# Kernel optimization log

Hardware: AMD Instinct MI355X
Metric: run time of the kernel (lower is better)

Reference implementation:

```python
import jax, jax.numpy as jnp
import numpy as np

CLASS_COUNT = 21
THRESHOLD = 0.5
ALPHA = 0.25
GAMMA = 2.0
VARIANCE = (0.1, 0.2)

B, A, N_OBJ = 32, 24576, 16


def point_form(boxes):
    # center form (cx, cy, w, h) -> point form (xmin, ymin, xmax, ymax)
    return jnp.concatenate([boxes[:, :2] - boxes[:, 2:] / 2,
                            boxes[:, :2] + boxes[:, 2:] / 2], axis=1)


def jaccard(truths, priors):
    # truths [N,4], priors [A,4] both in point form -> IoU [N, A]
    lt = jnp.maximum(truths[:, None, :2], priors[None, :, :2])
    rb = jnp.minimum(truths[:, None, 2:], priors[None, :, 2:])
    wh = jnp.clip(rb - lt, 0.0, None)
    inter = wh[..., 0] * wh[..., 1]
    area_t = ((truths[:, 2] - truths[:, 0]) * (truths[:, 3] - truths[:, 1]))[:, None]
    area_p = ((priors[:, 2] - priors[:, 0]) * (priors[:, 3] - priors[:, 1]))[None, :]
    return inter / (area_t + area_p - inter)


def match_one(labels, truths, anchors):
    # labels [N] int, truths [N,4] point form, anchors [A,4] center form
    overlaps = jaccard(truths, point_form(anchors))           # [N, A]
    best_prior_idx = jnp.argmax(overlaps, axis=1)             # [N]
    best_truth_overlap = jnp.max(overlaps, axis=0)            # [A]
    best_truth_idx = jnp.argmax(overlaps, axis=0)             # [A]
    # ensure every gt matches its best prior
    best_truth_overlap = best_truth_overlap.at[best_prior_idx].set(2.0)
    best_truth_idx = best_truth_idx.at[best_prior_idx].set(jnp.arange(truths.shape[0]))
    matches = truths[best_truth_idx]                          # [A, 4]
    conf = jnp.where(best_truth_overlap < THRESHOLD, 0, labels[best_truth_idx])
    # encode with variances
    g_cxcy = ((matches[:, :2] + matches[:, 2:]) * 0.5 - anchors[:, :2]) / (VARIANCE[0] * anchors[:, 2:])
    g_wh = jnp.log((matches[:, 2:] - matches[:, :2]) / anchors[:, 2:]) / VARIANCE[1]
    return conf, jnp.concatenate([g_cxcy, g_wh], axis=1)


def setup_inputs() -> dict:
    key = jax.random.key(0)
    k1, k2, k3, k4, k5, k6, k7 = jax.random.split(key, 7)
    class_preds = jax.random.normal(k1, (B, A, CLASS_COUNT), dtype=jnp.float32)
    loc_preds = jax.random.normal(k2, (B, A, 4), dtype=jnp.float32)
    # ground-truth boxes: random valid point-form boxes in [0,1]
    ctr = jax.random.uniform(k3, (B, N_OBJ, 2), minval=0.2, maxval=0.8)
    wh = jax.random.uniform(k4, (B, N_OBJ, 2), minval=0.05, maxval=0.3)
    loc_targets = jnp.clip(jnp.concatenate([ctr - wh / 2, ctr + wh / 2], axis=-1), 0.0, 1.0)
    class_targets = jax.random.randint(k5, (B, N_OBJ), 1, CLASS_COUNT)
    # anchors in center form
    a_ctr = jax.random.uniform(k6, (A, 2), minval=0.05, maxval=0.95)
    a_wh = jax.random.uniform(k7, (A, 2), minval=0.05, maxval=0.4)
    anchors = jnp.concatenate([a_ctr, a_wh], axis=1)
    return {"class_preds": class_preds, "loc_preds": loc_preds,
            "loc_targets": loc_targets, "anchors": anchors,
            "class_targets": class_targets}


def reference(class_preds, loc_preds, loc_targets, anchors, class_targets):
    conf, loc_t = jax.vmap(match_one, in_axes=(0, 0, None))(class_targets, loc_targets, anchors)
    pos = conf > 0                                            # [B, A]
    num_matched = jnp.sum(pos).astype(jnp.float32)
    # smooth L1 over positive anchors (sum reduction, beta=1)
    d = loc_preds - loc_t
    ad = jnp.abs(d)
    sl1 = jnp.where(ad < 1.0, 0.5 * d * d, ad - 0.5)
    loc_loss = jnp.sum(sl1 * pos[..., None].astype(sl1.dtype))
    # focal loss (drop background column 0)
    cp = class_preds.reshape(-1, CLASS_COUNT)[:, 1:]          # [B*A, C-1]
    t = jax.nn.one_hot(conf.reshape(-1), CLASS_COUNT, dtype=cp.dtype)[:, 1:]
    p = jax.nn.sigmoid(cp)
    pt = jnp.where(t > 0, p, 1.0 - p)
    w = (1.0 - pt) ** GAMMA
    w = jnp.where(t > 0, ALPHA * w, (1.0 - ALPHA) * w)
    # stable binary cross entropy with logits, weighted, sum reduction
    bce = jnp.maximum(cp, 0.0) - cp * t + jnp.log1p(jnp.exp(-jnp.abs(cp)))
    class_loss = jnp.sum(w * bce)
    class_loss = class_loss / num_matched
    loc_loss = loc_loss / num_matched
    return jnp.stack([class_loss, loc_loss, class_loss + loc_loss])
```

## Files before the change

### kernel.cpp

```cpp
#include <hip/hip_runtime.h>

#define A_COUNT 24576
#define B_COUNT 32
#define NOBJ 16
#define C_COUNT 21

#define NCH 96
#define CHUNK (A_COUNT / NCH)
#define NBLK (NCH * B_COUNT)
#define TOTAL4 (B_COUNT * A_COUNT * C_COUNT / 4)
#define STRIDE4 (NBLK * 256)

#define WS_BPP 0
#define WS_LOCP 393216
#define WS_CLSP 405504
#define WS_POSP 417792
#define WS_DLOC 430080
#define WS_DCLS 430208
#define WS_DPOS 430336

__device__ __forceinline__ unsigned long long pack_key(float iou, int a) {
    unsigned int ib = __float_as_uint(iou);
    return ((unsigned long long)ib << 32) | (unsigned long long)(0xFFFFFFFFu - (unsigned int)a);
}

__device__ __forceinline__ float iou_pf(float tx0, float ty0, float tx1, float ty1, float at,
                                        float x0, float y0, float x1, float y1, float ap) {
    float lx = fmaxf(tx0, x0), ly = fmaxf(ty0, y0);
    float rx = fminf(tx1, x1), ry = fminf(ty1, y1);
    float w = fmaxf(rx - lx, 0.0f), h = fmaxf(ry - ly, 0.0f);
    float inter = w * h;
    return inter * __builtin_amdgcn_rcpf(at + ap - inter);
}

__device__ __forceinline__ float sl1(float d) {
    float ad = fabsf(d);
    return (ad < 1.0f) ? 0.5f * d * d : ad - 0.5f;
}

__device__ __forceinline__ float loc_term(float4 t, float4 an, float4 lp) {
    float gx = ((t.x + t.z) * 0.5f - an.x) / (0.1f * an.z);
    float gy = ((t.y + t.w) * 0.5f - an.y) / (0.1f * an.w);
    float gw = __logf((t.z - t.x) / an.z) * 5.0f;
    float gh = __logf((t.w - t.y) / an.w) * 5.0f;
    return sl1(lp.x - gx) + sl1(lp.y - gy) + sl1(lp.z - gw) + sl1(lp.w - gh);
}

__device__ __forceinline__ float corr_term(float x) {
    float E = __expf(x);
    float den = 1.0f + E;
    float s = __builtin_amdgcn_rcpf(den);
    float p = E * s;
    float L = __logf(den);
    return 0.25f * s * s * (L - x) - 0.75f * p * p * L;
}

#define FOC(xval, rr, acc) {                                 \
    float E_ = __expf(xval);                                 \
    float den_ = 1.0f + E_;                                  \
    float s_ = __builtin_amdgcn_rcpf(den_);                  \
    float p_ = E_ * s_;                                      \
    float L_ = __logf(den_);                                 \
    float v_ = ((rr) == 0 || (rr) == 21) ? 0.0f : p_ * p_ * L_; \
    acc += v_; }

__global__ __launch_bounds__(256, 4) void k_main(const float* __restrict__ cls,
                                                 const float4* __restrict__ locp,
                                                 const float4* __restrict__ anchors,
                                                 const float4* __restrict__ truths,
                                                 const int* __restrict__ labels,
                                                 unsigned long long* __restrict__ bp_partial,
                                                 float* __restrict__ loc_partial,
                                                 float* __restrict__ cls_partial,
                                                 unsigned int* __restrict__ pos_partial) {
    const int ch = blockIdx.x;
    const int b = blockIdx.y;
    const int tid = threadIdx.x;
    __shared__ float4 s_t[NOBJ];
    __shared__ float s_area[NOBJ];
    __shared__ int s_lab[NOBJ];
    __shared__ unsigned long long s_keys[8][256];
    if (tid < NOBJ) {
        float4 t = truths[b * NOBJ + tid];
        s_t[tid] = t;
        s_area[tid] = (t.z - t.x) * (t.w - t.y);
        s_lab[tid] = labels[b * NOBJ + tid];
    }
    __syncthreads();
    const int a0 = ch * CHUNK + tid;
    float4 an0 = anchors[a0];
    float p0x0 = an0.x - an0.z * 0.5f, p0y0 = an0.y - an0.w * 0.5f;
    float p0x1 = an0.x + an0.z * 0.5f, p0y1 = an0.y + an0.w * 0.5f;
    float ap0 = (p0x1 - p0x0) * (p0y1 - p0y0);
    float best0 = -1.0f;
    int idx0 = 0;
#pragma unroll
    for (int half = 0; half < 2; ++half) {
#pragma unroll
        for (int n = 0; n < 8; ++n) {
            const int nt = half * 8 + n;
            float4 t = s_t[nt];
            float at = s_area[nt];
            float iou0 = iou_pf(t.x, t.y, t.z, t.w, at, p0x0, p0y0, p0x1, p0y1, ap0);
            if (iou0 > best0) { best0 = iou0; idx0 = nt; }
            s_keys[n][tid] = pack_key(iou0, a0);
        }
        __syncthreads();
        if (tid < 128) {
            const int g = tid >> 4, l = tid & 15;
            unsigned long long k = s_keys[g][l];
#pragma unroll
            for (int kk = 1; kk < 16; ++kk) {
                unsigned long long v = s_keys[g][l + 16 * kk];
                k = (v > k) ? v : k;
            }
#pragma unroll
            for (int s = 8; s >= 1; s >>= 1) {
                unsigned long long o = __shfl_xor(k, s);
                k = (o > k) ? o : k;
            }
            if (l == 0) bp_partial[(b * NOBJ + half * 8 + g) * NCH + ch] = k;
        }
        __syncthreads();
    }
    float loc_l = 0.0f, corr_acc = 0.0f;
    unsigned int pos = 0;
    if (!(best0 < 0.5f)) {
        pos = 1;
        loc_l = loc_term(s_t[idx0], an0, locp[(size_t)b * A_COUNT + a0]);
        corr_acc = corr_term(cls[((size_t)b * A_COUNT + a0) * C_COUNT + s_lab[idx0]]);
    }

    const int bid = b * NCH + ch;
    float cls_acc;
    {
        const float4* cls4 = (const float4*)cls;
        int i = bid * 256 + tid;
        unsigned int f = (unsigned int)i * 4u;
        unsigned int dq = f / 21u;
        int r = (int)(f - dq * 21u);
        float acc0 = 0.0f, acc1 = 0.0f, acc2 = 0.0f, acc3 = 0.0f;
        for (; i < TOTAL4; i += STRIDE4) {
            float4 x4 = cls4[i];
            FOC(x4.x, r + 0, acc0); FOC(x4.y, r + 1, acc1);
            FOC(x4.z, r + 2, acc2); FOC(x4.w, r + 3, acc3);
            r += 12; if (r >= 21) r -= 21;
        }
        cls_acc = corr_acc + 0.75f * ((acc0 + acc1) + (acc2 + acc3));
    }

#pragma unroll
    for (int s = 32; s >= 1; s >>= 1) {
        loc_l += __shfl_xor(loc_l, s);
        cls_acc += __shfl_xor(cls_acc, s);
        pos += __shfl_xor(pos, s);
    }
    __shared__ float s_ll[4], s_cl[4];
    __shared__ unsigned int s_pp[4];
    if ((tid & 63) == 0) {
        s_ll[tid >> 6] = loc_l;
        s_cl[tid >> 6] = cls_acc;
        s_pp[tid >> 6] = pos;
    }
    __syncthreads();
    if (tid == 0) {
        loc_partial[bid] = s_ll[0] + s_ll[1] + s_ll[2] + s_ll[3];
        cls_partial[bid] = s_cl[0] + s_cl[1] + s_cl[2] + s_cl[3];
        pos_partial[bid] = s_pp[0] + s_pp[1] + s_pp[2] + s_pp[3];
    }
}

__global__ __launch_bounds__(256) void k_fix(const float* __restrict__ cls,
                                             const float4* __restrict__ locp,
                                             const float4* __restrict__ anchors,
                                             const float4* __restrict__ truths,
                                             const int* __restrict__ labels,
                                             const unsigned long long* __restrict__ bp_partial,
                                             float* __restrict__ dloc,
                                             float* __restrict__ dcls,
                                             int* __restrict__ dpos) {
    const int b = blockIdx.x;
    const int tid = threadIdx.x;
    __shared__ int s_bp[NOBJ];
    {
        const int g = tid >> 4, l = tid & 15;
        const unsigned long long* pp = &bp_partial[(size_t)(b * NOBJ + g) * NCH];
        unsigned long long k = pp[l];
#pragma unroll
        for (int kk = 1; kk < 6; ++kk) {
            unsigned long long v = pp[l + 16 * kk];
            k = (v > k) ? v : k;
        }
#pragma unroll
        for (int s = 8; s >= 1; s >>= 1) {
            unsigned long long o = __shfl_xor(k, s);
            k = (o > k) ? o : k;
        }
        if (l == 0) {
            unsigned int ia = 0xFFFFFFFFu - (unsigned int)(k & 0xFFFFFFFFull);
            s_bp[g] = (ia >= A_COUNT) ? -1 : (int)ia;
        }
    }
    __syncthreads();
    float d_loc = 0.0f, d_cls = 0.0f;
    int d_pos = 0;
    if (tid < NOBJ) {
        const int n = tid;
        const int q = s_bp[n];
        bool winner = (q >= 0);
        for (int n2 = n + 1; n2 < NOBJ; ++n2)
            if (s_bp[n2] == q) winner = false;
        if (winner) {
            float4 an = anchors[q];
            float px0 = an.x - an.z * 0.5f, py0 = an.y - an.w * 0.5f;
            float px1 = an.x + an.z * 0.5f, py1 = an.y + an.w * 0.5f;
            float ap = (px1 - px0) * (py1 - py0);
            float best = -1.0f;
            int idx = 0;
            for (int n2 = 0; n2 < NOBJ; ++n2) {
                float4 t = truths[b * NOBJ + n2];
                float at = (t.z - t.x) * (t.w - t.y);
                float iou = iou_pf(t.x, t.y, t.z, t.w, at, px0, py0, px1, py1, ap);
                if (iou > best) { best = iou; idx = n2; }
            }
            float4 lp = locp[(size_t)b * A_COUNT + q];
            if (!(best < 0.5f)) {
                d_pos -= 1;
                d_loc -= loc_term(truths[b * NOBJ + idx], an, lp);
                d_cls -= corr_term(cls[((size_t)b * A_COUNT + q) * C_COUNT + labels[b * NOBJ + idx]]);
            }
            d_pos += 1;
            d_loc += loc_term(truths[b * NOBJ + n], an, lp);
            d_cls += corr_term(cls[((size_t)b * A_COUNT + q) * C_COUNT + labels[b * NOBJ + n]]);
        }
    }
    if (tid < 64) {
#pragma unroll
        for (int s = 8; s >= 1; s >>= 1) {
            d_loc += __shfl_xor(d_loc, s);
            d_cls += __shfl_xor(d_cls, s);
            d_pos += __shfl_xor(d_pos, s);
        }
        if (tid == 0) {
            dloc[b] = d_loc;
            dcls[b] = d_cls;
            dpos[b] = d_pos;
        }
    }
}

__global__ __launch_bounds__(256) void k_final(const float* __restrict__ loc_partial,
                                               const float* __restrict__ cls_partial,
                                               const unsigned int* __restrict__ pos_partial,
                                               const float* __restrict__ dloc,
                                               const float* __restrict__ dcls,
                                               const int* __restrict__ dpos,
                                               float* __restrict__ out) {
    const int tid = threadIdx.x;
    double loc = 0.0, clsv = 0.0;
    int pos = 0;
    for (int i = tid; i < NBLK; i += 256) {
        loc += (double)loc_partial[i];
        clsv += (double)cls_partial[i];
        pos += (int)pos_partial[i];
    }
    if (tid < B_COUNT) {
        loc += (double)dloc[tid];
        clsv += (double)dcls[tid];
        pos += dpos[tid];
    }
#pragma unroll
    for (int s = 32; s >= 1; s >>= 1) {
        loc += __shfl_xor(loc, s);
        clsv += __shfl_xor(clsv, s);
        pos += __shfl_xor(pos, s);
    }
    __shared__ double s_l[4], s_c[4];
    __shared__ int s_p[4];
    if ((tid & 63) == 0) {
        s_l[tid >> 6] = loc;
        s_c[tid >> 6] = clsv;
        s_p[tid >> 6] = pos;
    }
    __syncthreads();
    if (tid == 0) {
        double L = s_l[0] + s_l[1] + s_l[2] + s_l[3];
        double Cv = s_c[0] + s_c[1] + s_c[2] + s_c[3];
        float nm = (float)(s_p[0] + s_p[1] + s_p[2] + s_p[3]);
        float cf = (float)Cv / nm;
        float lf = (float)L / nm;
        out[0] = cf;
        out[1] = lf;
        out[2] = cf + lf;
    }
}

extern "C" void kernel_launch(void* const* d_in, const int* in_sizes, int n_in,
                              void* d_out, int out_size, void* d_ws, size_t ws_size,
                              hipStream_t stream) {
    const float* cls = (const float*)d_in[0];
    const float4* locp = (const float4*)d_in[1];
    const float4* truths = (const float4*)d_in[2];
    const float4* anchors = (const float4*)d_in[3];
    const int* labels = (const int*)d_in[4];

    char* ws = (char*)d_ws;
    unsigned long long* bp_partial = (unsigned long long*)(ws + WS_BPP);
    float* loc_partial = (float*)(ws + WS_LOCP);
    float* cls_partial = (float*)(ws + WS_CLSP);
    unsigned int* pos_partial = (unsigned int*)(ws + WS_POSP);
    float* dloc = (float*)(ws + WS_DLOC);
    float* dcls = (float*)(ws + WS_DCLS);
    int* dpos = (int*)(ws + WS_DPOS);

    k_main<<<dim3(NCH, B_COUNT), 256, 0, stream>>>(cls, locp, anchors, truths, labels,
                                                   bp_partial, loc_partial, cls_partial, pos_partial);
    k_fix<<<B_COUNT, 256, 0, stream>>>(cls, locp, anchors, truths, labels, bp_partial,
                                       dloc, dcls, dpos);
    k_final<<<1, 256, 0, stream>>>(loc_partial, cls_partial, pos_partial, dloc, dcls, dpos,
                                   (float*)d_out);
}
```

Before: 41.65 us.

## Replace shared-memory key reduction with wave shuffle argmax and raise occupancy

The per-truth best-anchor reduction, which staged 64-bit keys in a 16KB shared array with two barrier rounds per half, becomes a wavefront shuffle max plus ballot to pick the first lane holding the maximum. Each wave writes one key per truth to a small shared array and 16 threads combine the four waves. This removes most shared-memory traffic and barriers and shrinks LDS use, and launch bounds are raised to 8 blocks per SM to allow more occupancy. The lowest-lane tie break assumes lane order matches anchor order so the smallest anchor index wins, and the higher occupancy target may limit registers for the focal-loss loop.

```diff
diff --git a/kernel.cpp b/kernel.cpp
--- a/kernel.cpp
+++ b/kernel.cpp
@@ -64,7 +64,7 @@
     float v_ = ((rr) == 0 || (rr) == 21) ? 0.0f : p_ * p_ * L_; \
     acc += v_; }
 
-__global__ __launch_bounds__(256, 4) void k_main(const float* __restrict__ cls,
+__global__ __launch_bounds__(256, 8) void k_main(const float* __restrict__ cls,
                                                  const float4* __restrict__ locp,
                                                  const float4* __restrict__ anchors,
                                                  const float4* __restrict__ truths,
@@ -76,10 +76,11 @@
     const int ch = blockIdx.x;
     const int b = blockIdx.y;
     const int tid = threadIdx.x;
+    const int wv = tid >> 6, ln = tid & 63;
     __shared__ float4 s_t[NOBJ];
     __shared__ float s_area[NOBJ];
     __shared__ int s_lab[NOBJ];
-    __shared__ unsigned long long s_keys[8][256];
+    __shared__ unsigned long long s_w[NOBJ][4];
     if (tid < NOBJ) {
         float4 t = truths[b * NOBJ + tid];
         s_t[tid] = t;
@@ -95,33 +96,23 @@
     float best0 = -1.0f;
     int idx0 = 0;
 #pragma unroll
-    for (int half = 0; half < 2; ++half) {
-#pragma unroll
-        for (int n = 0; n < 8; ++n) {
-            const int nt = half * 8 + n;
-            float4 t = s_t[nt];
-            float at = s_area[nt];
-            float iou0 = iou_pf(t.x, t.y, t.z, t.w, at, p0x0, p0y0, p0x1, p0y1, ap0);
-            if (iou0 > best0) { best0 = iou0; idx0 = nt; }
-            s_keys[n][tid] = pack_key(iou0, a0);
-        }
-        __syncthreads();
-        if (tid < 128) {
-            const int g = tid >> 4, l = tid & 15;
-            unsigned long long k = s_keys[g][l];
-#pragma unroll
-            for (int kk = 1; kk < 16; ++kk) {
-                unsigned long long v = s_keys[g][l + 16 * kk];
-                k = (v > k) ? v : k;
-            }
-#pragma unroll
-            for (int s = 8; s >= 1; s >>= 1) {
-                unsigned long long o = __shfl_xor(k, s);
-                k = (o > k) ? o : k;
-            }
-            if (l == 0) bp_partial[(b * NOBJ + half * 8 + g) * NCH + ch] = k;
-        }
-        __syncthreads();
+    for (int n = 0; n < NOBJ; ++n) {
+        float4 t = s_t[n];
+        float iou = iou_pf(t.x, t.y, t.z, t.w, s_area[n], p0x0, p0y0, p0x1, p0y1, ap0);
+        if (iou > best0) { best0 = iou; idx0 = n; }
+        float m = iou;
+#pragma unroll
+        for (int s = 32; s >= 1; s >>= 1) m = fmaxf(m, __shfl_xor(m, s));
+        unsigned long long mask = __ballot(iou == m);
+        if (ln == __builtin_ctzll(mask))
+            s_w[n][wv] = pack_key(iou, a0);
+    }
+    __syncthreads();
+    if (tid < NOBJ) {
+        unsigned long long k = s_w[tid][0];
+#pragma unroll
+        for (int i = 1; i < 4; ++i) k = (s_w[tid][i] > k) ? s_w[tid][i] : k;
+        bp_partial[(b * NOBJ + tid) * NCH + ch] = k;
     }
     float loc_l = 0.0f, corr_acc = 0.0f;
     unsigned int pos = 0;
@@ -157,10 +148,10 @@
     }
     __shared__ float s_ll[4], s_cl[4];
     __shared__ unsigned int s_pp[4];
-    if ((tid & 63) == 0) {
-        s_ll[tid >> 6] = loc_l;
-        s_cl[tid >> 6] = cls_acc;
-        s_pp[tid >> 6] = pos;
+    if (ln == 0) {
+        s_ll[wv] = loc_l;
+        s_cl[wv] = cls_acc;
+        s_pp[wv] = pos;
     }
     __syncthreads();
     if (tid == 0) {
```

Measured after the change: 48.85 us. +17.3%, slower.

## Merge fix-up and final reduction into one tail kernel; prefetch focal loads

Applied to the files above, without the earlier changes.

Replaces the per-batch fix-up kernel and the final reduction kernel with a single one-block tail kernel. It performs the best-prior argmax for all 512 rows, applies the forced-match corrections, and sums all partials, which removes one kernel launch and the workspace round trip. The focal-loss streaming loop in the main kernel now software-prefetches the next float4 before computing on the current one, to hide load latency. The cost is that the fix-up work is serialized into a single block instead of 32.

```diff
diff --git a/kernel.cpp b/kernel.cpp
--- a/kernel.cpp
+++ b/kernel.cpp
@@ -8,6 +8,7 @@
 #define NCH 96
 #define CHUNK (A_COUNT / NCH)
 #define NBLK (NCH * B_COUNT)
+#define NROWS (B_COUNT * NOBJ)
 #define TOTAL4 (B_COUNT * A_COUNT * C_COUNT / 4)
 #define STRIDE4 (NBLK * 256)
 
@@ -15,9 +16,6 @@
 #define WS_LOCP 393216
 #define WS_CLSP 405504
 #define WS_POSP 417792
-#define WS_DLOC 430080
-#define WS_DCLS 430208
-#define WS_DPOS 430336
 
 __device__ __forceinline__ unsigned long long pack_key(float iou, int a) {
     unsigned int ib = __float_as_uint(iou);
@@ -140,10 +138,17 @@
         unsigned int dq = f / 21u;
         int r = (int)(f - dq * 21u);
         float acc0 = 0.0f, acc1 = 0.0f, acc2 = 0.0f, acc3 = 0.0f;
-        for (; i < TOTAL4; i += STRIDE4) {
-            float4 x4 = cls4[i];
-            FOC(x4.x, r + 0, acc0); FOC(x4.y, r + 1, acc1);
-            FOC(x4.z, r + 2, acc2); FOC(x4.w, r + 3, acc3);
+        float4 cur = cls4[i];
+        for (;;) {
+            const int inext = i + STRIDE4;
+            const bool more = inext < TOTAL4;
+            float4 nxt;
+            if (more) nxt = cls4[inext];
+            FOC(cur.x, r + 0, acc0); FOC(cur.y, r + 1, acc1);
+            FOC(cur.z, r + 2, acc2); FOC(cur.w, r + 3, acc3);
+            if (!more) break;
+            cur = nxt;
+            i = inext;
             r += 12; if (r >= 21) r -= 21;
         }
         cls_acc = corr_acc + 0.75f * ((acc0 + acc1) + (acc2 + acc3));
@@ -170,104 +175,80 @@
     }
 }
 
-__global__ __launch_bounds__(256) void k_fix(const float* __restrict__ cls,
-                                             const float4* __restrict__ locp,
-                                             const float4* __restrict__ anchors,
-                                             const float4* __restrict__ truths,
-                                             const int* __restrict__ labels,
-                                             const unsigned long long* __restrict__ bp_partial,
-                                             float* __restrict__ dloc,
-                                             float* __restrict__ dcls,
-                                             int* __restrict__ dpos) {
-    const int b = blockIdx.x;
+__global__ __launch_bounds__(256) void k_tail(const float* __restrict__ cls,
+                                              const float4* __restrict__ locp,
+                                              const float4* __restrict__ anchors,
+                                              const float4* __restrict__ truths,
+                                              const int* __restrict__ labels,
+                                              const unsigned long long* __restrict__ bp_partial,
+                                              const float* __restrict__ loc_partial,
+                                              const float* __restrict__ cls_partial,
+                                              const unsigned int* __restrict__ pos_partial,
+                                              float* __restrict__ out) {
     const int tid = threadIdx.x;
-    __shared__ int s_bp[NOBJ];
+    __shared__ int s_bp[NROWS];
     {
         const int g = tid >> 4, l = tid & 15;
-        const unsigned long long* pp = &bp_partial[(size_t)(b * NOBJ + g) * NCH];
-        unsigned long long k = pp[l];
-#pragma unroll
-        for (int kk = 1; kk < 6; ++kk) {
-            unsigned long long v = pp[l + 16 * kk];
-            k = (v > k) ? v : k;
-        }
-#pragma unroll
-        for (int s = 8; s >= 1; s >>= 1) {
-            unsigned long long o = __shfl_xor(k, s);
-            k = (o > k) ? o : k;
-        }
-        if (l == 0) {
-            unsigned int ia = 0xFFFFFFFFu - (unsigned int)(k & 0xFFFFFFFFull);
-            s_bp[g] = (ia >= A_COUNT) ? -1 : (int)ia;
-        }
-    }
-    __syncthreads();
+        for (int base = 0; base < NROWS; base += 16) {
+            const int row = base + g;
+            const unsigned long long* pp = &bp_partial[(size_t)row * NCH];
+            unsigned long long k = pp[l];
+#pragma unroll
+            for (int kk = 1; kk < 6; ++kk) {
+                unsigned long long v = pp[l + 16 * kk];
+                k = (v > k) ? v : k;
+            }
+#pragma unroll
+            for (int s = 8; s >= 1; s >>= 1) {
+                unsigned long long o = __shfl_xor(k, s);
+                k = (o > k) ? o : k;
+            }
+            if (l == 0) {
+                unsigned int ia = 0xFFFFFFFFu - (unsigned int)(k & 0xFFFFFFFFull);
+                s_bp[row] = (ia >= A_COUNT) ? -1 : (int)ia;
+            }
+        }
+    }
+    __syncthreads();
+
     float d_loc = 0.0f, d_cls = 0.0f;
     int d_pos = 0;
-    if (tid < NOBJ) {
-        const int n = tid;
-        const int q = s_bp[n];
+    for (int pr = tid; pr < NROWS; pr += 256) {
+        const int b2 = pr >> 4, n = pr & 15;
+        const int q = s_bp[pr];
         bool winner = (q >= 0);
         for (int n2 = n + 1; n2 < NOBJ; ++n2)
-            if (s_bp[n2] == q) winner = false;
-        if (winner) {
-            float4 an = anchors[q];
-            float px0 = an.x - an.z * 0.5f, py0 = an.y - an.w * 0.5f;
-            float px1 = an.x + an.z * 0.5f, py1 = an.y + an.w * 0.5f;
-            float ap = (px1 - px0) * (py1 - py0);
-            float best = -1.0f;
-            int idx = 0;
-            for (int n2 = 0; n2 < NOBJ; ++n2) {
-                float4 t = truths[b * NOBJ + n2];
-                float at = (t.z - t.x) * (t.w - t.y);
-                float iou = iou_pf(t.x, t.y, t.z, t.w, at, px0, py0, px1, py1, ap);
-                if (iou > best) { best = iou; idx = n2; }
-            }
-            float4 lp = locp[(size_t)b * A_COUNT + q];
-            if (!(best < 0.5f)) {
-                d_pos -= 1;
-                d_loc -= loc_term(truths[b * NOBJ + idx], an, lp);
-                d_cls -= corr_term(cls[((size_t)b * A_COUNT + q) * C_COUNT + labels[b * NOBJ + idx]]);
-            }
-            d_pos += 1;
-            d_loc += loc_term(truths[b * NOBJ + n], an, lp);
-            d_cls += corr_term(cls[((size_t)b * A_COUNT + q) * C_COUNT + labels[b * NOBJ + n]]);
-        }
-    }
-    if (tid < 64) {
-#pragma unroll
-        for (int s = 8; s >= 1; s >>= 1) {
-            d_loc += __shfl_xor(d_loc, s);
-            d_cls += __shfl_xor(d_cls, s);
-            d_pos += __shfl_xor(d_pos, s);
-        }
-        if (tid == 0) {
-            dloc[b] = d_loc;
-            dcls[b] = d_cls;
-            dpos[b] = d_pos;
-        }
-    }
-}
-
-__global__ __launch_bounds__(256) void k_final(const float* __restrict__ loc_partial,
-                                               const float* __restrict__ cls_partial,
-                                               const unsigned int* __restrict__ pos_partial,
-                                               const float* __restrict__ dloc,
-                                               const float* __restrict__ dcls,
-                                               const int* __restrict__ dpos,
-                                               float* __restrict__ out) {
-    const int tid = threadIdx.x;
-    double loc = 0.0, clsv = 0.0;
-    int pos = 0;
+            if (s_bp[(b2 << 4) | n2] == q) winner = false;
+        if (!winner) continue;
+        float4 an = anchors[q];
+        float px0 = an.x - an.z * 0.5f, py0 = an.y - an.w * 0.5f;
+        float px1 = an.x + an.z * 0.5f, py1 = an.y + an.w * 0.5f;
+        float ap = (px1 - px0) * (py1 - py0);
+        float best = -1.0f;
+        int idx = 0;
+        for (int n2 = 0; n2 < NOBJ; ++n2) {
+            float4 t = truths[b2 * NOBJ + n2];
+            float at = (t.z - t.x) * (t.w - t.y);
+            float iou = iou_pf(t.x, t.y, t.z, t.w, at, px0, py0, px1, py1, ap);
+            if (iou > best) { best = iou; idx = n2; }
+        }
+        float4 lp = locp[(size_t)b2 * A_COUNT + q];
+        if (!(best < 0.5f)) {
+            d_pos -= 1;
+            d_loc -= loc_term(truths[b2 * NOBJ + idx], an, lp);
+            d_cls -= corr_term(cls[((size_t)b2 * A_COUNT + q) * C_COUNT + labels[b2 * NOBJ + idx]]);
+        }
+        d_pos += 1;
+        d_loc += loc_term(truths[b2 * NOBJ + n], an, lp);
+        d_cls += corr_term(cls[((size_t)b2 * A_COUNT + q) * C_COUNT + labels[b2 * NOBJ + n]]);
+    }
+
+    double loc = (double)d_loc, clsv = (double)d_cls;
+    int pos = d_pos;
     for (int i = tid; i < NBLK; i += 256) {
         loc += (double)loc_partial[i];
         clsv += (double)cls_partial[i];
         pos += (int)pos_partial[i];
-    }
-    if (tid < B_COUNT) {
-        loc += (double)dloc[tid];
-        clsv += (double)dcls[tid];
-        pos += dpos[tid];
     }
 #pragma unroll
     for (int s = 32; s >= 1; s >>= 1) {
@@ -309,14 +290,9 @@
     float* loc_partial = (float*)(ws + WS_LOCP);
     float* cls_partial = (float*)(ws + WS_CLSP);
     unsigned int* pos_partial = (unsigned int*)(ws + WS_POSP);
-    float* dloc = (float*)(ws + WS_DLOC);
-    float* dcls = (float*)(ws + WS_DCLS);
-    int* dpos = (int*)(ws + WS_DPOS);
 
     k_main<<<dim3(NCH, B_COUNT), 256, 0, stream>>>(cls, locp, anchors, truths, labels,
                                                    bp_partial, loc_partial, cls_partial, pos_partial);
-    k_fix<<<B_COUNT, 256, 0, stream>>>(cls, locp, anchors, truths, labels, bp_partial,
-                                       dloc, dcls, dpos);
-    k_final<<<1, 256, 0, stream>>>(loc_partial, cls_partial, pos_partial, dloc, dcls, dpos,
-                                   (float*)d_out);
-}
+    k_tail<<<1, 256, 0, stream>>>(cls, locp, anchors, truths, labels, bp_partial,
+                                  loc_partial, cls_partial, pos_partial, (float*)d_out);
+}
```

Result: slower. 59.11 us (+41.9%).
